# Kernel optimization log

Measured on AMD Instinct MI355X. Metric: run time of the kernel, lower is better.

## Reference

```python
import jax, jax.numpy as jnp
import numpy as np

D, NH, NL, NP, NLAYERS, DFF = 256, 8, 4, 4, 6, 1024
DH = D // NH
SHAPES = [(96, 96), (48, 48), (24, 24), (12, 12)]
STARTS = np.concatenate([[0], np.cumsum([h * w for h, w in SHAPES])[:-1]]).tolist()
LQ = sum(h * w for h, w in SHAPES)
B = 2


def setup_inputs():
    ks = iter(jax.random.split(jax.random.key(0), 64))
    inp = {}
    for i, (h, w) in enumerate(SHAPES):
        inp[f"src{i}"] = jax.random.normal(next(ks), (B, D, h, w), jnp.float32)
        inp[f"pos{i}"] = jax.random.normal(next(ks), (B, D, h, w), jnp.float32) * 0.1
    inp["level_embed"] = jax.random.normal(next(ks), (NL, D), jnp.float32) * 0.02
    W = lambda s, sc: jax.random.normal(next(ks), s, jnp.float32) * sc
    inp["W_off"] = W((NLAYERS, D, NH * NL * NP * 2), 0.01)
    inp["b_off"] = W((NLAYERS, NH * NL * NP * 2), 0.5)
    inp["W_attn"] = W((NLAYERS, D, NH * NL * NP), 0.02)
    inp["b_attn"] = W((NLAYERS, NH * NL * NP), 0.02)
    inp["W_val"] = W((NLAYERS, D, D), 0.05)
    inp["b_val"] = jnp.zeros((NLAYERS, D), jnp.float32)
    inp["W_out"] = W((NLAYERS, D, D), 0.05)
    inp["b_out"] = jnp.zeros((NLAYERS, D), jnp.float32)
    inp["ln1_g"] = jnp.ones((NLAYERS, D), jnp.float32)
    inp["ln1_b"] = jnp.zeros((NLAYERS, D), jnp.float32)
    inp["W_ffn1"] = W((NLAYERS, D, DFF), 0.05)
    inp["b_ffn1"] = jnp.zeros((NLAYERS, DFF), jnp.float32)
    inp["W_ffn2"] = W((NLAYERS, DFF, D), 0.05)
    inp["b_ffn2"] = jnp.zeros((NLAYERS, D), jnp.float32)
    inp["ln2_g"] = jnp.ones((NLAYERS, D), jnp.float32)
    inp["ln2_b"] = jnp.zeros((NLAYERS, D), jnp.float32)
    return inp


def layer_norm(x, g, b):
    mu = x.mean(-1, keepdims=True)
    var = ((x - mu) ** 2).mean(-1, keepdims=True)
    return (x - mu) * jax.lax.rsqrt(var + 1e-5) * g + b


def reference_points():
    refs = []
    for h, w in SHAPES:
        ys = (jnp.arange(h, dtype=jnp.float32) + 0.5) / h
        xs = (jnp.arange(w, dtype=jnp.float32) + 0.5) / w
        gy, gx = jnp.meshgrid(ys, xs, indexing="ij")
        refs.append(jnp.stack([gx.reshape(-1), gy.reshape(-1)], -1))
    return jnp.concatenate(refs, 0)  # [LQ, 2] (x, y); valid_ratios==1 so level-independent


def bilinear(v, loc, H_, W_):
    # v: [B, H*W, NH, DH]; loc: [B, LQ, NH, NP, 2] normalized to [0,1]
    # matches F.grid_sample(mode='bilinear', padding_mode='zeros', align_corners=False)
    x = loc[..., 0] * W_ - 0.5
    y = loc[..., 1] * H_ - 0.5
    x0f, y0f = jnp.floor(x), jnp.floor(y)
    lx, ly = x - x0f, y - y0f
    x0, y0 = x0f.astype(jnp.int32), y0f.astype(jnp.int32)

    def g(xi, yi):
        valid = ((xi >= 0) & (xi < W_) & (yi >= 0) & (yi < H_)).astype(v.dtype)
        flat = jnp.clip(yi, 0, H_ - 1) * W_ + jnp.clip(xi, 0, W_ - 1)  # [B,LQ,NH,NP]
        idx = flat.transpose(0, 1, 3, 2).reshape(B, LQ * NP, NH)
        got = jnp.take_along_axis(v, jnp.broadcast_to(idx[..., None], (B, LQ * NP, NH, DH)), axis=1)
        got = got.reshape(B, LQ, NP, NH, DH).transpose(0, 1, 3, 2, 4)  # [B,LQ,NH,NP,DH]
        return got * valid[..., None]

    return (g(x0, y0) * ((1 - lx) * (1 - ly))[..., None]
            + g(x0 + 1, y0) * (lx * (1 - ly))[..., None]
            + g(x0, y0 + 1) * ((1 - lx) * ly)[..., None]
            + g(x0 + 1, y0 + 1) * (lx * ly)[..., None])


def reference(src0, src1, src2, src3, pos0, pos1, pos2, pos3, level_embed,
              W_off, b_off, W_attn, b_attn, W_val, b_val, W_out, b_out,
              ln1_g, ln1_b, W_ffn1, b_ffn1, W_ffn2, b_ffn2, ln2_g, ln2_b):
    srcs = [src0, src1, src2, src3]
    poss = [pos0, pos1, pos2, pos3]
    x = jnp.concatenate([s.reshape(B, D, -1).transpose(0, 2, 1) for s in srcs], 1)  # [B,LQ,D]
    pos = jnp.concatenate(
        [p.reshape(B, D, -1).transpose(0, 2, 1) + level_embed[i][None, None] for i, p in enumerate(poss)], 1)
    ref = reference_points()  # [LQ,2]
    norm = jnp.array([[w, h] for h, w in SHAPES], jnp.float32)  # [NL,2] = (W,H)

    for li in range(NLAYERS):
        q = x + pos
        off = (q @ W_off[li] + b_off[li]).reshape(B, LQ, NH, NL, NP, 2)
        attn = jax.nn.softmax((q @ W_attn[li] + b_attn[li]).reshape(B, LQ, NH, NL * NP), -1)
        attn = attn.reshape(B, LQ, NH, NL, NP)
        val = (x @ W_val[li] + b_val[li]).reshape(B, LQ, NH, DH)
        loc = ref[None, :, None, None, None, :] + off / norm[None, None, None, :, None, :]
        out = jnp.zeros((B, LQ, NH, DH), x.dtype)
        for l, (h, w) in enumerate(SHAPES):
            vl = val[:, STARTS[l]:STARTS[l] + h * w]
            sampled = bilinear(vl, loc[:, :, :, l], h, w)  # [B,LQ,NH,NP,DH]
            out = out + (sampled * attn[:, :, :, l, :, None]).sum(3)
        out = out.reshape(B, LQ, D) @ W_out[li] + b_out[li]
        x = layer_norm(x + out, ln1_g[li], ln1_b[li])
        ffn = jax.nn.relu(x @ W_ffn1[li] + b_ffn1[li]) @ W_ffn2[li] + b_ffn2[li]
        x = layer_norm(x + ffn, ln2_g[li], ln2_b[li])
    return x
```

## Files before the change

### kernel.cpp

```cpp
#include <hip/hip_runtime.h>
#include <stdint.h>

#define NHEAD  8
#define NLAYER 6
#define BATCH  2
#define LQ     12240
#define MTOK   (BATCH*LQ)
#define MPAD   24576

typedef __attribute__((ext_vector_type(8))) short bf16x8;
typedef __attribute__((ext_vector_type(4))) float f32x4;
typedef __attribute__((ext_vector_type(4))) short s16x4;

__device__ __forceinline__ unsigned short f2bf(float f) {
  union { float f; uint32_t u; } v; v.f = f;
  uint32_t u = v.u;
  uint32_t r = (u + 0x7fffu + ((u >> 16) & 1u)) >> 16;
  return (unsigned short)r;
}
__device__ __forceinline__ float bf2f(unsigned short s) {
  union { uint32_t u; float f; } v; v.u = ((uint32_t)s) << 16;
  return v.f;
}
__device__ __forceinline__ void gll16(const unsigned short* g, unsigned short* l) {
  __builtin_amdgcn_global_load_lds(
      (const __attribute__((address_space(1))) uint32_t*)g,
      (__attribute__((address_space(3))) uint32_t*)l, 16, 0, 0);
}

template<int EPI, int BM>
__global__ __launch_bounds__(256)
void gemm_kernel(const unsigned short* __restrict__ A,
                 const unsigned short* __restrict__ BT,
                 const float* __restrict__ bias,
                 float* __restrict__ Cf,
                 unsigned short* __restrict__ Cb,
                 int K, int ldc)
{
  constexpr int MT = BM / 32;
  __shared__ unsigned short lA[BM*64];
  __shared__ unsigned short lB[128*64];
  const int tid  = threadIdx.x;
  const int lane = tid & 63;
  const int wm = ((tid >> 6) >> 1) * (BM/2);
  const int wn = ((tid >> 6) & 1) * 64;
  const size_t row0 = (size_t)blockIdx.x * BM;
  const size_t col0 = (size_t)blockIdx.y * 128;

  f32x4 acc[MT][4] = {};

  for (int kt = 0; kt < K; kt += 64) {
#pragma unroll
    for (int i = 0; i < MT; ++i) {
      const int slot = i*256 + tid;
      const int r  = slot >> 3;
      const int cs = (slot & 7) ^ (r & 7);
      gll16(A + (row0 + r) * (size_t)K + kt + cs*8, &lA[slot*8]);
    }
#pragma unroll
    for (int i = 0; i < 4; ++i) {
      const int slot = i*256 + tid;
      const int r  = slot >> 3;
      const int cs = (slot & 7) ^ (r & 7);
      gll16(BT + (col0 + r) * (size_t)K + kt + cs*8, &lB[slot*8]);
    }
    __syncthreads();
#pragma unroll
    for (int kk = 0; kk < 2; ++kk) {
      bf16x8 af[MT], bfv[4];
#pragma unroll
      for (int m = 0; m < MT; ++m) {
        const int r  = wm + m*16 + (lane & 15);
        const int ch = (kk*4 + (lane >> 4)) ^ (r & 7);
        af[m] = *(const bf16x8*)(&lA[r*64 + ch*8]);
      }
#pragma unroll
      for (int n = 0; n < 4; ++n) {
        const int r  = wn + n*16 + (lane & 15);
        const int ch = (kk*4 + (lane >> 4)) ^ (r & 7);
        bfv[n] = *(const bf16x8*)(&lB[r*64 + ch*8]);
      }
#pragma unroll
      for (int m = 0; m < MT; ++m)
#pragma unroll
        for (int n = 0; n < 4; ++n)
          acc[m][n] = __builtin_amdgcn_mfma_f32_16x16x32_bf16(af[m], bfv[n], acc[m][n], 0, 0, 0);
    }
    __syncthreads();
  }

  const int lq = lane >> 4;
  const int lr = lane & 15;
#pragma unroll
  for (int n = 0; n < 4; ++n) {
    const int col = (int)col0 + wn + n*16 + lr;
    const float bv = bias ? bias[col] : 0.f;
#pragma unroll
    for (int m = 0; m < MT; ++m) {
      const size_t rb = row0 + wm + m*16 + lq*4;
#pragma unroll
      for (int i = 0; i < 4; ++i) {
        float v = acc[m][n][i] + bv;
        if (EPI == 2) v = fmaxf(v, 0.f);
        if (EPI == 0) Cf[(rb + i) * (size_t)ldc + col] = v;
        else          Cb[(rb + i) * (size_t)ldc + col] = f2bf(v);
      }
    }
  }
}

template<int MODE>
__global__ __launch_bounds__(512)
void gemm_ln_kernel(const unsigned short* __restrict__ A,
                    const unsigned short* __restrict__ BT,
                    const float* __restrict__ bias,
                    const unsigned short* __restrict__ xresbf,
                    const float* __restrict__ g,
                    const float* __restrict__ bn,
                    const unsigned short* __restrict__ posbf,
                    unsigned short* __restrict__ xbf,
                    unsigned short* __restrict__ qbf,
                    float* __restrict__ dout,
                    int K)
{
  __shared__ unsigned short lA[64*64];
  __shared__ unsigned short lB[256*64];
  __shared__ float rs1[4][64];
  __shared__ float rs2[4][64];
  const int tid  = threadIdx.x;
  const int lane = tid & 63;
  const int w    = tid >> 6;
  const int wr   = w >> 2;
  const int wc   = w & 3;
  const size_t row0 = (size_t)blockIdx.x * 64;

  f32x4 acc[2][4] = {};

  for (int kt = 0; kt < K; kt += 64) {
    {
      const int slot = tid;
      const int r  = slot >> 3;
      const int cs = (slot & 7) ^ (r & 7);
      gll16(A + (row0 + r) * (size_t)K + kt + cs*8, &lA[slot*8]);
    }
#pragma unroll
    for (int i = 0; i < 4; ++i) {
      const int slot = i*512 + tid;
      const int r  = slot >> 3;
      const int cs = (slot & 7) ^ (r & 7);
      gll16(BT + (size_t)r * K + kt + cs*8, &lB[slot*8]);
    }
    __syncthreads();
#pragma unroll
    for (int kk = 0; kk < 2; ++kk) {
      bf16x8 af[2], bfv[4];
#pragma unroll
      for (int m = 0; m < 2; ++m) {
        const int r  = wr*32 + m*16 + (lane & 15);
        const int ch = (kk*4 + (lane >> 4)) ^ (r & 7);
        af[m] = *(const bf16x8*)(&lA[r*64 + ch*8]);
      }
#pragma unroll
      for (int n = 0; n < 4; ++n) {
        const int r  = wc*64 + n*16 + (lane & 15);
        const int ch = (kk*4 + (lane >> 4)) ^ (r & 7);
        bfv[n] = *(const bf16x8*)(&lB[r*64 + ch*8]);
      }
#pragma unroll
      for (int m = 0; m < 2; ++m)
#pragma unroll
        for (int n = 0; n < 4; ++n)
          acc[m][n] = __builtin_amdgcn_mfma_f32_16x16x32_bf16(af[m], bfv[n], acc[m][n], 0, 0, 0);
    }
    __syncthreads();
  }

  const int lq = lane >> 4;
  const int lr = lane & 15;
  float bcol[4], gcol[4], bncol[4];
#pragma unroll
  for (int n = 0; n < 4; ++n) {
    const int c = wc*64 + n*16 + lr;
    bcol[n]  = bias[c];
    gcol[n]  = g[c];
    bncol[n] = bn[c];
  }
#pragma unroll
  for (int m = 0; m < 2; ++m)
#pragma unroll
    for (int i = 0; i < 4; ++i) {
      const size_t row = row0 + wr*32 + m*16 + lq*4 + i;
#pragma unroll
      for (int n = 0; n < 4; ++n)
        acc[m][n][i] += bcol[n] + bf2f(xresbf[row*256 + wc*64 + n*16 + lr]);
    }
#pragma unroll
  for (int m = 0; m < 2; ++m)
#pragma unroll
    for (int i = 0; i < 4; ++i) {
      float t1 = acc[m][0][i] + acc[m][1][i] + acc[m][2][i] + acc[m][3][i];
      float t2 = acc[m][0][i]*acc[m][0][i] + acc[m][1][i]*acc[m][1][i]
               + acc[m][2][i]*acc[m][2][i] + acc[m][3][i]*acc[m][3][i];
#pragma unroll
      for (int o = 1; o < 16; o <<= 1) {
        t1 += __shfl_xor(t1, o, 64);
        t2 += __shfl_xor(t2, o, 64);
      }
      if (lr == 0) {
        rs1[wc][wr*32 + m*16 + lq*4 + i] = t1;
        rs2[wc][wr*32 + m*16 + lq*4 + i] = t2;
      }
    }
  __syncthreads();
#pragma unroll
  for (int m = 0; m < 2; ++m)
#pragma unroll
    for (int i = 0; i < 4; ++i) {
      const int r = wr*32 + m*16 + lq*4 + i;
      const float s1 = rs1[0][r] + rs1[1][r] + rs1[2][r] + rs1[3][r];
      const float s2 = rs2[0][r] + rs2[1][r] + rs2[2][r] + rs2[3][r];
      const float mu  = s1 * (1.f/256.f);
      const float var = s2 * (1.f/256.f) - mu*mu;
      const float rstd = rsqrtf(var + 1e-5f);
      const size_t row = row0 + r;
#pragma unroll
      for (int n = 0; n < 4; ++n) {
        const int c = wc*64 + n*16 + lr;
        const float nv = (acc[m][n][i] - mu) * rstd * gcol[n] + bncol[n];
        const size_t idx = row*256 + c;
        if (MODE == 2) {
          if (row < MTOK) dout[idx] = nv;
        } else {
          xbf[idx] = f2bf(nv);
          if (MODE == 1) qbf[idx] = f2bf(nv + bf2f(posbf[idx]));
        }
      }
    }
}

__global__ void pack_kernel(const float* __restrict__ s0, const float* __restrict__ s1,
                            const float* __restrict__ s2, const float* __restrict__ s3,
                            const float* __restrict__ p0, const float* __restrict__ p1,
                            const float* __restrict__ p2, const float* __restrict__ p3,
                            const float* __restrict__ lev,
                            unsigned short* __restrict__ xo, unsigned short* __restrict__ po)
{
  const int bt = blockIdx.x;
  int lvl, st;
  if      (bt < 288) { lvl = 0; st = bt; }
  else if (bt < 360) { lvl = 1; st = bt - 288; }
  else if (bt < 378) { lvl = 2; st = bt - 360; }
  else               { lvl = 3; st = bt - 378; }
  const int HWs[4] = {9216, 2304, 576, 144};
  const int LSs[4] = {0, 9216, 11520, 12096};
  const int hw = HWs[lvl], ls = LSs[lvl];
  const int b = blockIdx.z & 1, isp = blockIdx.z >> 1;
  const float* ins[8] = {s0, s1, s2, s3, p0, p1, p2, p3};
  const float* in = ins[isp*4 + lvl];
  const int sbase = st*32, d0 = blockIdx.y*32;
  __shared__ float tile[32][33];
  const int tx = threadIdx.x, ty = threadIdx.y;
#pragma unroll
  for (int j = 0; j < 4; ++j) {
    int ss = sbase + tx;
    int dd = d0 + ty + j*8;
    tile[ty + j*8][tx] = (ss < hw) ? in[((size_t)b*256 + dd)*hw + ss] : 0.f;
  }
  __syncthreads();
  const float addv = isp ? lev[lvl*256 + d0 + tx] : 0.f;
  unsigned short* outp = isp ? po : xo;
#pragma unroll
  for (int j = 0; j < 4; ++j) {
    int ss = sbase + ty + j*8;
    if (ss < hw)
      outp[(size_t)(b*LQ + ls + ss)*256 + d0 + tx] = f2bf(tile[tx][ty + j*8] + addv);
  }
}

__global__ void wtrans_kernel(const float* __restrict__ Woff, const float* __restrict__ Watt,
                              const float* __restrict__ Wval, const float* __restrict__ Wout,
                              const float* __restrict__ Wf1,  const float* __restrict__ Wf2,
                              unsigned short* __restrict__ WoaT, unsigned short* __restrict__ WvalT,
                              unsigned short* __restrict__ WoutT, unsigned short* __restrict__ Wf1T,
                              unsigned short* __restrict__ Wf2T)
{
  const int li = blockIdx.z;
  const int bt = blockIdx.x;
  const float* in; unsigned short* out; int Kd, Nd, tn, tIdx;
  if      (bt < 64)  { in = Woff + (size_t)li*65536;  out = WoaT  + (size_t)li*98304;         Kd=256;  Nd=256;  tn=8;  tIdx=bt; }
  else if (bt < 96)  { in = Watt + (size_t)li*32768;  out = WoaT  + (size_t)li*98304 + 65536; Kd=256;  Nd=128;  tn=4;  tIdx=bt-64; }
  else if (bt < 160) { in = Wval + (size_t)li*65536;  out = WvalT + (size_t)li*65536;         Kd=256;  Nd=256;  tn=8;  tIdx=bt-96; }
  else if (bt < 224) { in = Wout + (size_t)li*65536;  out = WoutT + (size_t)li*65536;         Kd=256;  Nd=256;  tn=8;  tIdx=bt-160; }
  else if (bt < 480) { in = Wf1  + (size_t)li*262144; out = Wf1T  + (size_t)li*262144;        Kd=256;  Nd=1024; tn=32; tIdx=bt-224; }
  else               { in = Wf2  + (size_t)li*262144; out = Wf2T  + (size_t)li*262144;        Kd=1024; Nd=256;  tn=8;  tIdx=bt-480; }
  const int kt = tIdx / tn, nt = tIdx - kt*tn;
  const int k0 = kt*32, n0 = nt*32;
  __shared__ float tile[32][33];
  const int tx = threadIdx.x, ty = threadIdx.y;
#pragma unroll
  for (int j = 0; j < 4; ++j)
    tile[ty + j*8][tx] = in[(size_t)(k0 + ty + j*8) * Nd + n0 + tx];
  __syncthreads();
#pragma unroll
  for (int j = 0; j < 4; ++j)
    out[(size_t)(n0 + ty + j*8) * Kd + k0 + tx] = f2bf(tile[tx][ty + j*8]);
}

__global__ void bias_concat_kernel(const float* __restrict__ boff, const float* __restrict__ batt,
                                   float* __restrict__ boa)
{
  const int li = blockIdx.x, i = threadIdx.x;
  boa[li*384 + i] = (i < 256) ? boff[li*256 + i] : batt[li*128 + (i - 256)];
}

__global__ void prep_kernel(unsigned short* __restrict__ xbf,
                            const unsigned short* __restrict__ posbf,
                            unsigned short* __restrict__ qbf)
{
  const int idx = blockIdx.x * 256 + threadIdx.x;
  const int row = idx >> 6;
  if (row < MTOK) {
    const s16x4 xv = *(const s16x4*)(xbf + (size_t)idx*4);
    const s16x4 pv = *(const s16x4*)(posbf + (size_t)idx*4);
    s16x4 qb;
#pragma unroll
    for (int j = 0; j < 4; ++j)
      qb[j] = (short)f2bf(bf2f((unsigned short)xv[j]) + bf2f((unsigned short)pv[j]));
    *(s16x4*)(qbf + (size_t)idx*4) = qb;
  } else {
    const s16x4 z = {};
    *(s16x4*)(xbf + (size_t)idx*4) = z;
    *(s16x4*)(qbf + (size_t)idx*4) = z;
  }
}

__global__ __launch_bounds__(256)
void sample_kernel(const unsigned short* __restrict__ Coab, const float* __restrict__ valf,
                   unsigned short* __restrict__ outbf)
{
  __shared__ int4  pdo[32][17];
  __shared__ f32x4 pdw[32][17];
  const int tid = threadIdx.x;
  const int gi  = tid >> 3;
  const int g   = blockIdx.x * 32 + gi;
  const int t   = g >> 3, h = g & 7;
  const int b   = (t >= LQ) ? 1 : 0;

  {
    const int i0 = tid & 7;
    int4  ov0 = {0,0,0,0}, ov1 = {0,0,0,0};
    f32x4 wv0 = {0,0,0,0}, wv1 = {0,0,0,0};
    if (t < MTOK) {
      const int q = t - b * LQ;
      float refx, refy;
      if      (q < 9216)  { const int r = q;         const int rw = r/96; refx = (r - rw*96 + 0.5f)*(1.f/96.f); refy = (rw + 0.5f)*(1.f/96.f); }
      else if (q < 11520) { const int r = q - 9216;  const int rw = r/48; refx = (r - rw*48 + 0.5f)*(1.f/48.f); refy = (rw + 0.5f)*(1.f/48.f); }
      else if (q < 12096) { const int r = q - 11520; const int rw = r/24; refx = (r - rw*24 + 0.5f)*(1.f/24.f); refy = (rw + 0.5f)*(1.f/24.f); }
      else                { const int r = q - 12096; const int rw = r/12; refx = (r - rw*12 + 0.5f)*(1.f/12.f); refy = (rw + 0.5f)*(1.f/12.f); }
      const size_t crow = (size_t)t * 384;
      const float l0 = bf2f(Coab[crow + 256 + h*16 + i0]);
      const float l1 = bf2f(Coab[crow + 256 + h*16 + i0 + 8]);
      float mx = fmaxf(l0, l1);
#pragma unroll
      for (int m = 1; m < 8; m <<= 1) mx = fmaxf(mx, __shfl_xor(mx, m, 64));
      const float e0 = __expf(l0 - mx), e1 = __expf(l1 - mx);
      float sum = e0 + e1;
#pragma unroll
      for (int m = 1; m < 8; m <<= 1) sum += __shfl_xor(sum, m, 64);
      const float inv = 1.f / sum;

      auto mkpd = [&](int i, float aw, int4& ov, f32x4& wv) {
        const int l    = i >> 2;
        const int wl   = (l == 0) ? 96 : (l == 1) ? 48 : (l == 2) ? 24 : 12;
        const int base = (l == 0) ? 0  : (l == 1) ? 9216 : (l == 2) ? 11520 : 12096;
        const float ox = bf2f(Coab[crow + h*32 + 2*i]);
        const float oy = bf2f(Coab[crow + h*32 + 2*i + 1]);
        const float fw = (float)wl;
        const float xx = refx*fw + ox - 0.5f;
        const float yy = refy*fw + oy - 0.5f;
        const float xf = floorf(xx), yf = floorf(yy);
        const int x0 = (int)xf, y0 = (int)yf;
        const float lx = xx - xf, ly = yy - yf;
        const bool vx0 = (x0   >= 0) & (x0   < wl);
        const bool vx1 = (x0+1 >= 0) & (x0+1 < wl);
        const bool vy0 = (y0   >= 0) & (y0   < wl);
        const bool vy1 = (y0+1 >= 0) & (y0+1 < wl);
        const int cx0 = min(max(x0,   0), wl-1);
        const int cx1 = min(max(x0+1, 0), wl-1);
        const int cy0 = min(max(y0,   0), wl-1);
        const int cy1 = min(max(y0+1, 0), wl-1);
        ov.x = (base + cy0*wl + cx0) * 1024;
        ov.y = (base + cy0*wl + cx1) * 1024;
        ov.z = (base + cy1*wl + cx0) * 1024;
        ov.w = (base + cy1*wl + cx1) * 1024;
        wv[0] = (vx0 & vy0) ? (1.f-lx)*(1.f-ly)*aw : 0.f;
        wv[1] = (vx1 & vy0) ? lx*(1.f-ly)*aw       : 0.f;
        wv[2] = (vx0 & vy1) ? (1.f-lx)*ly*aw       : 0.f;
        wv[3] = (vx1 & vy1) ? lx*ly*aw             : 0.f;
      };
      mkpd(i0,     e0 * inv, ov0, wv0);
      mkpd(i0 + 8, e1 * inv, ov1, wv1);
    }
    pdo[gi][i0]     = ov0;  pdw[gi][i0]     = wv0;
    pdo[gi][i0 + 8] = ov1;  pdw[gi][i0 + 8] = wv1;
  }
  __syncthreads();

  const int lane8 = tid & 7;
  const char* vb = (const char*)(valf + (size_t)b*LQ*256 + h*32 + lane8*4);
  const int4*  po8 = pdo[gi];
  const f32x4* pw8 = pdw[gi];
  f32x4 a0 = {}, a1 = {}, a2 = {}, a3 = {};
#pragma unroll
  for (int p = 0; p < 16; ++p) {
    const int4  o = po8[p];
    const f32x4 w = pw8[p];
    const f32x4 c0 = *(const f32x4*)(vb + o.x);
    const f32x4 c1 = *(const f32x4*)(vb + o.y);
    const f32x4 c2 = *(const f32x4*)(vb + o.z);
    const f32x4 c3 = *(const f32x4*)(vb + o.w);
    a0 += c0 * w[0];
    a1 += c1 * w[1];
    a2 += c2 * w[2];
    a3 += c3 * w[3];
  }
  const f32x4 s = (a0 + a1) + (a2 + a3);
  s16x4 ob;
#pragma unroll
  for (int j = 0; j < 4; ++j) ob[j] = (short)f2bf(s[j]);
  *(s16x4*)(outbf + (size_t)t*256 + h*32 + lane8*4) = ob;
}

extern "C" void kernel_launch(void* const* d_in, const int* in_sizes, int n_in,
                              void* d_out, int out_size, void* d_ws, size_t ws_size,
                              hipStream_t stream)
{
  const float* src0 = (const float*)d_in[0];
  const float* pos0 = (const float*)d_in[1];
  const float* src1 = (const float*)d_in[2];
  const float* pos1 = (const float*)d_in[3];
  const float* src2 = (const float*)d_in[4];
  const float* pos2 = (const float*)d_in[5];
  const float* src3 = (const float*)d_in[6];
  const float* pos3 = (const float*)d_in[7];
  const float* lev  = (const float*)d_in[8];
  const float* W_off= (const float*)d_in[9];
  const float* b_off= (const float*)d_in[10];
  const float* W_att= (const float*)d_in[11];
  const float* b_att= (const float*)d_in[12];
  const float* W_val= (const float*)d_in[13];
  const float* b_val= (const float*)d_in[14];
  const float* W_out= (const float*)d_in[15];
  const float* b_out= (const float*)d_in[16];
  const float* ln1g = (const float*)d_in[17];
  const float* ln1b = (const float*)d_in[18];
  const float* W_f1 = (const float*)d_in[19];
  const float* b_f1 = (const float*)d_in[20];
  const float* W_f2 = (const float*)d_in[21];
  const float* b_f2 = (const float*)d_in[22];
  const float* ln2g = (const float*)d_in[23];
  const float* ln2b = (const float*)d_in[24];

  char* wp = (char*)d_ws;
  auto take = [&](size_t bytes) { char* p = wp; wp += (bytes + 255) & ~(size_t)255; return p; };
  float* valf = (float*)take((size_t)MPAD*256*4);
  unsigned short* posbf  = (unsigned short*)take((size_t)MPAD*256*2);
  unsigned short* Coab   = (unsigned short*)take((size_t)MPAD*384*2);
  unsigned short* xbf    = (unsigned short*)take((size_t)MPAD*256*2);
  unsigned short* qbf    = (unsigned short*)take((size_t)MPAD*256*2);
  unsigned short* sampbf = (unsigned short*)take((size_t)MPAD*256*2);
  unsigned short* h1bf   = (unsigned short*)take((size_t)MPAD*1024*2);
  unsigned short* WoaT   = (unsigned short*)take((size_t)NLAYER*384*256*2);
  unsigned short* WvalT  = (unsigned short*)take((size_t)NLAYER*256*256*2);
  unsigned short* WoutT  = (unsigned short*)take((size_t)NLAYER*256*256*2);
  unsigned short* Wf1T   = (unsigned short*)take((size_t)NLAYER*1024*256*2);
  unsigned short* Wf2T   = (unsigned short*)take((size_t)NLAYER*256*1024*2);
  float* boa  = (float*)take((size_t)NLAYER*384*4);

  dim3 tb(32, 8);
  pack_kernel<<<dim3(383, 8, 4), tb, 0, stream>>>(src0, src1, src2, src3,
                                                  pos0, pos1, pos2, pos3, lev, xbf, posbf);
  wtrans_kernel<<<dim3(736, 1, 6), tb, 0, stream>>>(W_off, W_att, W_val, W_out, W_f1, W_f2,
                                                    WoaT, WvalT, WoutT, Wf1T, Wf2T);
  bias_concat_kernel<<<NLAYER, 384, 0, stream>>>(b_off, b_att, boa);
  prep_kernel<<<MPAD/4, 256, 0, stream>>>(xbf, posbf, qbf);

  for (int li = 0; li < NLAYER; ++li) {
    gemm_kernel<1,64><<<dim3(MPAD/64, 3), 256, 0, stream>>>(qbf, WoaT + (size_t)li*98304,
        boa + li*384, nullptr, Coab, 256, 384);
    gemm_kernel<0,64><<<dim3(MPAD/64, 2), 256, 0, stream>>>(xbf, WvalT + (size_t)li*65536,
        b_val + li*256, valf, nullptr, 256, 256);
    sample_kernel<<<MPAD/4, 256, 0, stream>>>(Coab, valf, sampbf);
    gemm_ln_kernel<0><<<MPAD/64, 512, 0, stream>>>(sampbf, WoutT + (size_t)li*65536,
        b_out + li*256, xbf, ln1g + li*256, ln1b + li*256, nullptr,
        xbf, nullptr, nullptr, 256);
    gemm_kernel<2,128><<<dim3(MPAD/128, 8), 256, 0, stream>>>(xbf, Wf1T + (size_t)li*262144,
        b_f1 + li*1024, nullptr, h1bf, 256, 1024);
    if (li < NLAYER-1)
      gemm_ln_kernel<1><<<MPAD/64, 512, 0, stream>>>(h1bf, Wf2T + (size_t)li*262144,
          b_f2 + li*256, xbf, ln2g + li*256, ln2b + li*256, posbf,
          xbf, qbf, nullptr, 1024);
    else
      gemm_ln_kernel<2><<<MPAD/64, 512, 0, stream>>>(h1bf, Wf2T + (size_t)li*262144,
          b_f2 + li*256, xbf, ln2g + li*256, ln2b + li*256, nullptr,
          nullptr, nullptr, (float*)d_out, 1024);
  }
}
```

Measured before the change: 905.0 us.

## Merge offset/attention and value projections into one GEMM launch; swizzle sample block order

The separate offset/attention projection GEMM and value projection GEMM are replaced by a single kernel. Its grid y-dimension selects which operand, weights, bias and output each block uses, which removes one launch per layer and lets both projections share the GPU concurrently. Separately, the sampling kernel remaps block indices so that consecutive blocks are spread across strided token ranges, intended to change cache and locality behaviour. The remap may hurt locality in value reads, and the fused kernel hard-codes K=256 and a 64x128 tile.

Measured after the change: 888.8 us. About the same (-1.8%).

```diff
diff --git a/kernel.cpp b/kernel.cpp
--- a/kernel.cpp
+++ b/kernel.cpp
@@ -104,6 +104,92 @@
         if (EPI == 2) v = fmaxf(v, 0.f);
         if (EPI == 0) Cf[(rb + i) * (size_t)ldc + col] = v;
         else          Cb[(rb + i) * (size_t)ldc + col] = f2bf(v);
+      }
+    }
+  }
+}
+
+__global__ __launch_bounds__(256)
+void gemm_qv_kernel(const unsigned short* __restrict__ qbf,
+                    const unsigned short* __restrict__ xbf,
+                    const unsigned short* __restrict__ WoaT_l,
+                    const unsigned short* __restrict__ WvalT_l,
+                    const float* __restrict__ boa_l,
+                    const float* __restrict__ bval_l,
+                    unsigned short* __restrict__ Coab,
+                    float* __restrict__ valf)
+{
+  __shared__ unsigned short lA[64*64];
+  __shared__ unsigned short lB[128*64];
+  const bool isq = blockIdx.y < 3;
+  const unsigned short* A  = isq ? qbf : xbf;
+  const unsigned short* BT = isq ? WoaT_l : WvalT_l;
+  const float* bias = isq ? boa_l : bval_l;
+  const int ldc  = isq ? 384 : 256;
+  const int colb = isq ? (int)blockIdx.y * 128 : ((int)blockIdx.y - 3) * 128;
+
+  const int tid  = threadIdx.x;
+  const int lane = tid & 63;
+  const int wm = ((tid >> 6) >> 1) * 32;
+  const int wn = ((tid >> 6) & 1) * 64;
+  const size_t row0 = (size_t)blockIdx.x * 64;
+
+  f32x4 acc[2][4] = {};
+
+  for (int kt = 0; kt < 256; kt += 64) {
+#pragma unroll
+    for (int i = 0; i < 2; ++i) {
+      const int slot = i*256 + tid;
+      const int r  = slot >> 3;
+      const int cs = (slot & 7) ^ (r & 7);
+      gll16(A + (row0 + r) * 256 + kt + cs*8, &lA[slot*8]);
+    }
+#pragma unroll
+    for (int i = 0; i < 4; ++i) {
+      const int slot = i*256 + tid;
+      const int r  = slot >> 3;
+      const int cs = (slot & 7) ^ (r & 7);
+      gll16(BT + (size_t)(colb + r) * 256 + kt + cs*8, &lB[slot*8]);
+    }
+    __syncthreads();
+#pragma unroll
+    for (int kk = 0; kk < 2; ++kk) {
+      bf16x8 af[2], bfv[4];
+#pragma unroll
+      for (int m = 0; m < 2; ++m) {
+        const int r  = wm + m*16 + (lane & 15);
+        const int ch = (kk*4 + (lane >> 4)) ^ (r & 7);
+        af[m] = *(const bf16x8*)(&lA[r*64 + ch*8]);
+      }
+#pragma unroll
+      for (int n = 0; n < 4; ++n) {
+        const int r  = wn + n*16 + (lane & 15);
+        const int ch = (kk*4 + (lane >> 4)) ^ (r & 7);
+        bfv[n] = *(const bf16x8*)(&lB[r*64 + ch*8]);
+      }
+#pragma unroll
+      for (int m = 0; m < 2; ++m)
+#pragma unroll
+        for (int n = 0; n < 4; ++n)
+          acc[m][n] = __builtin_amdgcn_mfma_f32_16x16x32_bf16(af[m], bfv[n], acc[m][n], 0, 0, 0);
+    }
+    __syncthreads();
+  }
+
+  const int lq = lane >> 4;
+  const int lr = lane & 15;
+#pragma unroll
+  for (int n = 0; n < 4; ++n) {
+    const int col = colb + wn + n*16 + lr;
+    const float bv = bias[col];
+#pragma unroll
+    for (int m = 0; m < 2; ++m) {
+      const size_t rb = row0 + wm + m*16 + lq*4;
+#pragma unroll
+      for (int i = 0; i < 4; ++i) {
+        const float v = acc[m][n][i] + bv;
+        if (isq) Coab[(rb + i) * 384 + col] = f2bf(v);
+        else     valf[(rb + i) * 256 + col] = v;
       }
     }
   }
@@ -342,7 +428,9 @@
   __shared__ f32x4 pdw[32][17];
   const int tid = threadIdx.x;
   const int gi  = tid >> 3;
-  const int g   = blockIdx.x * 32 + gi;
+  const int bid = blockIdx.x;
+  const int swz = (bid & 7) * ((MPAD/4) >> 3) + (bid >> 3);
+  const int g   = swz * 32 + gi;
   const int t   = g >> 3, h = g & 7;
   const int b   = (t >= LQ) ? 1 : 0;
 
@@ -486,10 +574,9 @@
   prep_kernel<<<MPAD/4, 256, 0, stream>>>(xbf, posbf, qbf);
 
   for (int li = 0; li < NLAYER; ++li) {
-    gemm_kernel<1,64><<<dim3(MPAD/64, 3), 256, 0, stream>>>(qbf, WoaT + (size_t)li*98304,
-        boa + li*384, nullptr, Coab, 256, 384);
-    gemm_kernel<0,64><<<dim3(MPAD/64, 2), 256, 0, stream>>>(xbf, WvalT + (size_t)li*65536,
-        b_val + li*256, valf, nullptr, 256, 256);
+    gemm_qv_kernel<<<dim3(MPAD/64, 5), 256, 0, stream>>>(qbf, xbf,
+        WoaT + (size_t)li*98304, WvalT + (size_t)li*65536,
+        boa + li*384, b_val + li*256, Coab, valf);
     sample_kernel<<<MPAD/4, 256, 0, stream>>>(Coab, valf, sampbf);
     gemm_ln_kernel<0><<<MPAD/64, 512, 0, stream>>>(sampbf, WoutT + (size_t)li*65536,
         b_out + li*256, xbf, ln1g + li*256, ln1b + li*256, nullptr,
```
